# Optimization experiments

Measured on AMD Instinct MI355X. Metric: run time of the kernel, lower is better.

Reference implementation:

```python
import jax, jax.numpy as jnp
import numpy as np

F = 39          # total fields = 13 numeric + 26 categorical
NUM_NUM = 13
N_CAT = 26
V = 100000      # vocab per categorical field
E = 16          # embed size
RED = max(1, F // 3)  # SE reduction size = 13
P = F * (F - 1) // 2  # 741 pairs
HID = [1024, 512, 256]
B = 4096

I_IDX, J_IDX = np.triu_indices(F, k=1)  # static pair indices, len P


def setup_inputs() -> dict:
    key = jax.random.key(0)
    ks = jax.random.split(key, 16)
    s = 0.01
    inp = {
        "cat": jax.random.randint(ks[0], (B, N_CAT), 0, V),
        "num": jax.random.normal(ks[1], (B, NUM_NUM), dtype=jnp.float32),
        "embed_tables": jax.random.normal(ks[2], (N_CAT, V, E), dtype=jnp.float32) * s,
        "num_emb": jax.random.normal(ks[3], (NUM_NUM, E), dtype=jnp.float32) * s,
        "W_se1": jax.random.normal(ks[4], (F, RED), dtype=jnp.float32) * 0.1,
        "W_se2": jax.random.normal(ks[5], (RED, F), dtype=jnp.float32) * 0.1,
        "W_bil": jax.random.normal(ks[6], (F, E, E), dtype=jnp.float32) * 0.1,  # per-field Linear(E,E,no bias), [field,in,out]
        "W_d1": jax.random.normal(ks[7], (2 * P * E, HID[0]), dtype=jnp.float32) * 0.01,
        "b_d1": jnp.zeros((HID[0],), dtype=jnp.float32),
        "W_d2": jax.random.normal(ks[8], (HID[0], HID[1]), dtype=jnp.float32) * 0.02,
        "b_d2": jnp.zeros((HID[1],), dtype=jnp.float32),
        "W_d3": jax.random.normal(ks[9], (HID[1], HID[2]), dtype=jnp.float32) * 0.02,
        "b_d3": jnp.zeros((HID[2],), dtype=jnp.float32),
        "W_out": jax.random.normal(ks[10], (HID[2], 1), dtype=jnp.float32) * 0.02,
        "b_out": jnp.zeros((1,), dtype=jnp.float32),
    }
    return inp


def _bilinear_each(x, W_bil):
    # x: [B,F,E]; project each field with its own matrix, then pairwise multiply.
    proj = jnp.einsum("bfe,fed->bfd", x, W_bil)            # [B,F,E]
    return proj[:, I_IDX, :] * x[:, J_IDX, :]               # [B,P,E]


def reference(cat, num, embed_tables, num_emb, W_se1, W_se2, W_bil,
              W_d1, b_d1, W_d2, b_d2, W_d3, b_d3, W_out, b_out):
    # categorical embeddings: per-field gather -> [B, N_CAT, E]
    cat_embed = embed_tables[jnp.arange(N_CAT)[None, :], cat]
    # numerical "embeddings": value * learned vector -> [B, NUM_NUM, E]
    num_embed = num[:, :, None] * num_emb[None, :, :]
    x = jnp.concatenate([num_embed, cat_embed], axis=1)     # [B,F,E]

    # SENET gating
    Z = jnp.mean(x, axis=-1)                                 # [B,F]
    A = jax.nn.relu(jax.nn.relu(Z @ W_se1) @ W_se2)          # [B,F]
    V = x * A[:, :, None]

    se_bi = _bilinear_each(V, W_bil)                         # [B,P,E]
    bi = _bilinear_each(x, W_bil)                            # [B,P,E]
    hid = jnp.concatenate([se_bi, bi], axis=1).reshape(x.shape[0], -1)  # [B, 2*P*E]

    h = jax.nn.relu(hid @ W_d1 + b_d1)
    h = jax.nn.relu(h @ W_d2 + b_d2)
    h = jax.nn.relu(h @ W_d3 + b_d3)
    return h @ W_out + b_out                                 # [B,1]
```

## Files before the change

### kernel.cpp

```cpp
#include <hip/hip_runtime.h>

typedef unsigned short u16;
typedef __attribute__((ext_vector_type(8))) __bf16 bf16x8;
typedef __attribute__((ext_vector_type(4))) float f32x4;

#define NF    39
#define NNUM  13
#define NCAT  26
#define VOC   100000
#define NPAIR 741
#define KHID  23712
#define BATCH 4096
#define HD1   1024
#define HD2   512
#define HD3   256

__device__ __forceinline__ u16 f2bf(float f) {
  unsigned u = __builtin_bit_cast(unsigned, f);
  return (u16)((u + 0x7fffu + ((u >> 16) & 1u)) >> 16);
}

__device__ __forceinline__ void gload16(const void* g, void* l) {
  __builtin_amdgcn_global_load_lds((const __attribute__((address_space(1))) void*)g,
                                   (__attribute__((address_space(3))) void*)l, 16, 0, 0);
}

__global__ __launch_bounds__(256) void fuse_front(
    const int* __restrict__ cat, const float* __restrict__ num,
    const float* __restrict__ tables, const float* __restrict__ nemb,
    const float* __restrict__ Wse1, const float* __restrict__ Wse2,
    const float* __restrict__ Wbil, u16* __restrict__ hid)
{
  __shared__ float xs[NF][16];
  __shared__ float wb[NF][16][16];
  __shared__ float pr[NF][16];
  __shared__ float Zs[NF], Ts[NNUM], As[NF];
  __shared__ unsigned char pis[NPAIR], pjs[NPAIR];

  const int b = blockIdx.x;
  const int tid = threadIdx.x;

  for (int i = tid; i < NF * 256; i += 256) ((float*)wb)[i] = Wbil[i];

  for (int t = tid; t < NNUM * 16; t += 256) {
    int f = t >> 4, e = t & 15;
    xs[f][e] = num[b * NNUM + f] * nemb[t];
  }
  for (int t = tid; t < NCAT * 16; t += 256) {
    int c = t >> 4, e = t & 15;
    int cv = cat[b * NCAT + c];
    xs[NNUM + c][e] = tables[((size_t)c * VOC + cv) * 16 + e];
  }
  for (int p = tid; p < NPAIR; p += 256) {
    int i = 0, rs = 0;
    while (p >= rs + (NF - 1 - i)) { rs += NF - 1 - i; ++i; }
    pis[p] = (unsigned char)i;
    pjs[p] = (unsigned char)(i + 1 + (p - rs));
  }
  __syncthreads();

  if (tid < NF) {
    float s = 0.f;
    #pragma unroll
    for (int e = 0; e < 16; ++e) s += xs[tid][e];
    Zs[tid] = s * (1.f / 16.f);
  }
  __syncthreads();
  if (tid < NNUM) {
    float s = 0.f;
    for (int f = 0; f < NF; ++f) s += Zs[f] * Wse1[f * NNUM + tid];
    Ts[tid] = fmaxf(s, 0.f);
  }
  __syncthreads();
  if (tid < NF) {
    float s = 0.f;
    for (int r = 0; r < NNUM; ++r) s += Ts[r] * Wse2[r * NF + tid];
    As[tid] = fmaxf(s, 0.f);
  }
  for (int t = tid; t < NF * 16; t += 256) {
    int f = t >> 4, d = t & 15;
    float s = 0.f;
    #pragma unroll
    for (int e = 0; e < 16; ++e) s += xs[f][e] * wb[f][e][d];
    pr[f][d] = s;
  }
  __syncthreads();

  u16* hr = hid + (size_t)b * KHID;
  for (int idx = tid; idx < NPAIR * 16; idx += 256) {
    int p = idx >> 4, e = idx & 15;
    int i = pis[p], j = pjs[p];
    float bv = pr[i][e] * xs[j][e];
    hr[NPAIR * 16 + idx] = f2bf(bv);
    hr[idx] = f2bf(As[i] * As[j] * bv);
  }
}

__global__ __launch_bounds__(256) void transpose_cast(
    const float* __restrict__ in, u16* __restrict__ out, int K, int N)
{
  __shared__ float t[32][33];
  const int k0 = blockIdx.x * 32, n0 = blockIdx.y * 32;
  const int c = threadIdx.x & 31, r = threadIdx.x >> 5;
  #pragma unroll
  for (int it = 0; it < 4; ++it)
    t[r + it * 8][c] = in[(size_t)(k0 + r + it * 8) * N + n0 + c];
  __syncthreads();
  #pragma unroll
  for (int it = 0; it < 4; ++it)
    out[(size_t)(n0 + r + it * 8) * K + k0 + c] = f2bf(t[c][r + it * 8]);
}

__global__ __launch_bounds__(512, 2) void gemm8p_bf16(
    const u16* __restrict__ A, const u16* __restrict__ Bt,
    float* __restrict__ Cp, int M, int N, int K, int totku, int kpb)
{
  __shared__ __align__(16) u16 lds[65536];

  const int tid = threadIdx.x;
  const int wid = tid >> 6, lane = tid & 63;

  const int d = blockIdx.x;
  const int x = d & 7, jj = d >> 3;
  const int mb = ((x & 3) << 2) | (jj & 3);
  const int nb = (jj >> 2) & 3;
  const int sb = ((x >> 2) << 1) | (jj >> 4);

  const int ks0 = sb * kpb;
  const int kunits = (totku - ks0 < kpb) ? (totku - ks0) : kpb;
  const int ftiles = kunits >> 1;

  const int wm = wid >> 2, wn = wid & 3;
  const int lrow = lane & 15, c0 = lane >> 4;

  const int rr = tid >> 2, cc = tid & 3, csrc = cc ^ ((rr >> 1) & 3);
  const u16* pAg = A  + (size_t)((size_t)mb * 256 + rr) * K + (size_t)ks0 * 32 + csrc * 8;
  const u16* pBg = Bt + (size_t)((size_t)nb * 256 + rr) * K + (size_t)ks0 * 32 + csrc * 8;
  const size_t rsk = (size_t)128 * K;
  const int dstoff = tid * 8;

  int offA[8], offB[4];
  #pragma unroll
  for (int m = 0; m < 8; ++m) {
    int r = wm * 128 + m * 16 + lrow;
    offA[m] = r * 32 + ((c0 ^ ((r >> 1) & 3)) << 3);
  }
  #pragma unroll
  for (int n = 0; n < 4; ++n) {
    int r = wn * 64 + n * 16 + lrow;
    offB[n] = r * 32 + ((c0 ^ ((r >> 1) & 3)) << 3);
  }

#define STAGE_A(g) { int sg = ((g) < kunits) ? (g) : (kunits - 1);          \
    const u16* s_ = pAg + (size_t)sg * 32;                                   \
    u16* dp_ = lds + (((g) & 3) * 8192) + dstoff;                            \
    gload16(s_, dp_); gload16(s_ + rsk, dp_ + 4096); }
#define STAGE_B(g) { int sg = ((g) < kunits) ? (g) : (kunits - 1);          \
    const u16* s_ = pBg + (size_t)sg * 32;                                   \
    u16* dp_ = lds + 32768 + (((g) & 3) * 8192) + dstoff;                    \
    gload16(s_, dp_); gload16(s_ + rsk, dp_ + 4096); }

  f32x4 acc[8][4];
  #pragma unroll
  for (int m = 0; m < 8; ++m)
    #pragma unroll
    for (int n = 0; n < 4; ++n) acc[m][n] = f32x4{0.f, 0.f, 0.f, 0.f};

  STAGE_A(0); STAGE_B(0); STAGE_A(1); STAGE_B(1); STAGE_A(2); STAGE_B(2); STAGE_B(3);
  asm volatile("s_waitcnt vmcnt(10)" ::: "memory");
  __builtin_amdgcn_s_barrier();

  bf16x8 a0, a1, a2, a3, bg0, bg1, bg2, bg3;

  for (int tt = 0; tt < ftiles; ++tt) {
    const int g0 = tt << 1;
    const u16* As0 = lds + ((g0 & 3) * 8192);
    const u16* As1 = lds + (((g0 + 1) & 3) * 8192);
    const u16* Bs0 = lds + 32768 + ((g0 & 3) * 8192);
    const u16* Bs1 = lds + 32768 + (((g0 + 1) & 3) * 8192);

    a0 = *reinterpret_cast<const bf16x8*>(As0 + offA[0]);
    a1 = *reinterpret_cast<const bf16x8*>(As0 + offA[1]);
    a2 = *reinterpret_cast<const bf16x8*>(As0 + offA[2]);
    a3 = *reinterpret_cast<const bf16x8*>(As0 + offA[3]);
    bg0 = *reinterpret_cast<const bf16x8*>(Bs0 + offB[0]);
    bg1 = *reinterpret_cast<const bf16x8*>(Bs0 + offB[1]);
    bg2 = *reinterpret_cast<const bf16x8*>(Bs0 + offB[2]);
    bg3 = *reinterpret_cast<const bf16x8*>(Bs0 + offB[3]);
    STAGE_A(g0 + 3);
    __builtin_amdgcn_sched_barrier(0);
    __builtin_amdgcn_s_barrier();
    asm volatile("s_waitcnt lgkmcnt(0)" ::: "memory");
    __builtin_amdgcn_sched_barrier(0);
    __builtin_amdgcn_s_setprio(1);
    acc[0][0] = __builtin_amdgcn_mfma_f32_16x16x32_bf16(a0, bg0, acc[0][0], 0, 0, 0);
    acc[0][1] = __builtin_amdgcn_mfma_f32_16x16x32_bf16(a0, bg1, acc[0][1], 0, 0, 0);
    acc[0][2] = __builtin_amdgcn_mfma_f32_16x16x32_bf16(a0, bg2, acc[0][2], 0, 0, 0);
    acc[0][3] = __builtin_amdgcn_mfma_f32_16x16x32_bf16(a0, bg3, acc[0][3], 0, 0, 0);
    acc[1][0] = __builtin_amdgcn_mfma_f32_16x16x32_bf16(a1, bg0, acc[1][0], 0, 0, 0);
    acc[1][1] = __builtin_amdgcn_mfma_f32_16x16x32_bf16(a1, bg1, acc[1][1], 0, 0, 0);
    acc[1][2] = __builtin_amdgcn_mfma_f32_16x16x32_bf16(a1, bg2, acc[1][2], 0, 0, 0);
    acc[1][3] = __builtin_amdgcn_mfma_f32_16x16x32_bf16(a1, bg3, acc[1][3], 0, 0, 0);
    acc[2][0] = __builtin_amdgcn_mfma_f32_16x16x32_bf16(a2, bg0, acc[2][0], 0, 0, 0);
    acc[2][1] = __builtin_amdgcn_mfma_f32_16x16x32_bf16(a2, bg1, acc[2][1], 0, 0, 0);
    acc[2][2] = __builtin_amdgcn_mfma_f32_16x16x32_bf16(a2, bg2, acc[2][2], 0, 0, 0);
    acc[2][3] = __builtin_amdgcn_mfma_f32_16x16x32_bf16(a2, bg3, acc[2][3], 0, 0, 0);
    acc[3][0] = __builtin_amdgcn_mfma_f32_16x16x32_bf16(a3, bg0, acc[3][0], 0, 0, 0);
    acc[3][1] = __builtin_amdgcn_mfma_f32_16x16x32_bf16(a3, bg1, acc[3][1], 0, 0, 0);
    acc[3][2] = __builtin_amdgcn_mfma_f32_16x16x32_bf16(a3, bg2, acc[3][2], 0, 0, 0);
    acc[3][3] = __builtin_amdgcn_mfma_f32_16x16x32_bf16(a3, bg3, acc[3][3], 0, 0, 0);
    __builtin_amdgcn_s_setprio(0);
    __builtin_amdgcn_sched_barrier(0);
    __builtin_amdgcn_s_barrier();

    a0 = *reinterpret_cast<const bf16x8*>(As0 + offA[4]);
    a1 = *reinterpret_cast<const bf16x8*>(As0 + offA[5]);
    a2 = *reinterpret_cast<const bf16x8*>(As0 + offA[6]);
    a3 = *reinterpret_cast<const bf16x8*>(As0 + offA[7]);
    STAGE_B(g0 + 4);
    __builtin_amdgcn_sched_barrier(0);
    __builtin_amdgcn_s_barrier();
    asm volatile("s_waitcnt lgkmcnt(0)" ::: "memory");
    __builtin_amdgcn_sched_barrier(0);
    __builtin_amdgcn_s_setprio(1);
    acc[4][0] = __builtin_amdgcn_mfma_f32_16x16x32_bf16(a0, bg0, acc[4][0], 0, 0, 0);
    acc[4][1] = __builtin_amdgcn_mfma_f32_16x16x32_bf16(a0, bg1, acc[4][1], 0, 0, 0);
    acc[4][2] = __builtin_amdgcn_mfma_f32_16x16x32_bf16(a0, bg2, acc[4][2], 0, 0, 0);
    acc[4][3] = __builtin_amdgcn_mfma_f32_16x16x32_bf16(a0, bg3, acc[4][3], 0, 0, 0);
    acc[5][0] = __builtin_amdgcn_mfma_f32_16x16x32_bf16(a1, bg0, acc[5][0], 0, 0, 0);
    acc[5][1] = __builtin_amdgcn_mfma_f32_16x16x32_bf16(a1, bg1, acc[5][1], 0, 0, 0);
    acc[5][2] = __builtin_amdgcn_mfma_f32_16x16x32_bf16(a1, bg2, acc[5][2], 0, 0, 0);
    acc[5][3] = __builtin_amdgcn_mfma_f32_16x16x32_bf16(a1, bg3, acc[5][3], 0, 0, 0);
    acc[6][0] = __builtin_amdgcn_mfma_f32_16x16x32_bf16(a2, bg0, acc[6][0], 0, 0, 0);
    acc[6][1] = __builtin_amdgcn_mfma_f32_16x16x32_bf16(a2, bg1, acc[6][1], 0, 0, 0);
    acc[6][2] = __builtin_amdgcn_mfma_f32_16x16x32_bf16(a2, bg2, acc[6][2], 0, 0, 0);
    acc[6][3] = __builtin_amdgcn_mfma_f32_16x16x32_bf16(a2, bg3, acc[6][3], 0, 0, 0);
    acc[7][0] = __builtin_amdgcn_mfma_f32_16x16x32_bf16(a3, bg0, acc[7][0], 0, 0, 0);
    acc[7][1] = __builtin_amdgcn_mfma_f32_16x16x32_bf16(a3, bg1, acc[7][1], 0, 0, 0);
    acc[7][2] = __builtin_amdgcn_mfma_f32_16x16x32_bf16(a3, bg2, acc[7][2], 0, 0, 0);
    acc[7][3] = __builtin_amdgcn_mfma_f32_16x16x32_bf16(a3, bg3, acc[7][3], 0, 0, 0);
    __builtin_amdgcn_s_setprio(0);
    __builtin_amdgcn_sched_barrier(0);
    asm volatile("s_waitcnt vmcnt(8)" ::: "memory");
    __builtin_amdgcn_s_barrier();

    a0 = *reinterpret_cast<const bf16x8*>(As1 + offA[0]);
    a1 = *reinterpret_cast<const bf16x8*>(As1 + offA[1]);
    a2 = *reinterpret_cast<const bf16x8*>(As1 + offA[2]);
    a3 = *reinterpret_cast<const bf16x8*>(As1 + offA[3]);
    bg0 = *reinterpret_cast<const bf16x8*>(Bs1 + offB[0]);
    bg1 = *reinterpret_cast<const bf16x8*>(Bs1 + offB[1]);
    bg2 = *reinterpret_cast<const bf16x8*>(Bs1 + offB[2]);
    bg3 = *reinterpret_cast<const bf16x8*>(Bs1 + offB[3]);
    STAGE_A(g0 + 4);
    __builtin_amdgcn_sched_barrier(0);
    __builtin_amdgcn_s_barrier();
    asm volatile("s_waitcnt lgkmcnt(0)" ::: "memory");
    __builtin_amdgcn_sched_barrier(0);
    __builtin_amdgcn_s_setprio(1);
    acc[0][0] = __builtin_amdgcn_mfma_f32_16x16x32_bf16(a0, bg0, acc[0][0], 0, 0, 0);
    acc[0][1] = __builtin_amdgcn_mfma_f32_16x16x32_bf16(a0, bg1, acc[0][1], 0, 0, 0);
    acc[0][2] = __builtin_amdgcn_mfma_f32_16x16x32_bf16(a0, bg2, acc[0][2], 0, 0, 0);
    acc[0][3] = __builtin_amdgcn_mfma_f32_16x16x32_bf16(a0, bg3, acc[0][3], 0, 0, 0);
    acc[1][0] = __builtin_amdgcn_mfma_f32_16x16x32_bf16(a1, bg0, acc[1][0], 0, 0, 0);
    acc[1][1] = __builtin_amdgcn_mfma_f32_16x16x32_bf16(a1, bg1, acc[1][1], 0, 0, 0);
    acc[1][2] = __builtin_amdgcn_mfma_f32_16x16x32_bf16(a1, bg2, acc[1][2], 0, 0, 0);
    acc[1][3] = __builtin_amdgcn_mfma_f32_16x16x32_bf16(a1, bg3, acc[1][3], 0, 0, 0);
    acc[2][0] = __builtin_amdgcn_mfma_f32_16x16x32_bf16(a2, bg0, acc[2][0], 0, 0, 0);
    acc[2][1] = __builtin_amdgcn_mfma_f32_16x16x32_bf16(a2, bg1, acc[2][1], 0, 0, 0);
    acc[2][2] = __builtin_amdgcn_mfma_f32_16x16x32_bf16(a2, bg2, acc[2][2], 0, 0, 0);
    acc[2][3] = __builtin_amdgcn_mfma_f32_16x16x32_bf16(a2, bg3, acc[2][3], 0, 0, 0);
    acc[3][0] = __builtin_amdgcn_mfma_f32_16x16x32_bf16(a3, bg0, acc[3][0], 0, 0, 0);
    acc[3][1] = __builtin_amdgcn_mfma_f32_16x16x32_bf16(a3, bg1, acc[3][1], 0, 0, 0);
    acc[3][2] = __builtin_amdgcn_mfma_f32_16x16x32_bf16(a3, bg2, acc[3][2], 0, 0, 0);
    acc[3][3] = __builtin_amdgcn_mfma_f32_16x16x32_bf16(a3, bg3, acc[3][3], 0, 0, 0);
    __builtin_amdgcn_s_setprio(0);
    __builtin_amdgcn_sched_barrier(0);
    __builtin_amdgcn_s_barrier();

    a0 = *reinterpret_cast<const bf16x8*>(As1 + offA[4]);
    a1 = *reinterpret_cast<const bf16x8*>(As1 + offA[5]);
    a2 = *reinterpret_cast<const bf16x8*>(As1 + offA[6]);
    a3 = *reinterpret_cast<const bf16x8*>(As1 + offA[7]);
    STAGE_B(g0 + 5);
    __builtin_amdgcn_sched_barrier(0);
    __builtin_amdgcn_s_barrier();
    asm volatile("s_waitcnt lgkmcnt(0)" ::: "memory");
    __builtin_amdgcn_sched_barrier(0);
    __builtin_amdgcn_s_setprio(1);
    acc[4][0] = __builtin_amdgcn_mfma_f32_16x16x32_bf16(a0, bg0, acc[4][0], 0, 0, 0);
    acc[4][1] = __builtin_amdgcn_mfma_f32_16x16x32_bf16(a0, bg1, acc[4][1], 0, 0, 0);
    acc[4][2] = __builtin_amdgcn_mfma_f32_16x16x32_bf16(a0, bg2, acc[4][2], 0, 0, 0);
    acc[4][3] = __builtin_amdgcn_mfma_f32_16x16x32_bf16(a0, bg3, acc[4][3], 0, 0, 0);
    acc[5][0] = __builtin_amdgcn_mfma_f32_16x16x32_bf16(a1, bg0, acc[5][0], 0, 0, 0);
    acc[5][1] = __builtin_amdgcn_mfma_f32_16x16x32_bf16(a1, bg1, acc[5][1], 0, 0, 0);
    acc[5][2] = __builtin_amdgcn_mfma_f32_16x16x32_bf16(a1, bg2, acc[5][2], 0, 0, 0);
    acc[5][3] = __builtin_amdgcn_mfma_f32_16x16x32_bf16(a1, bg3, acc[5][3], 0, 0, 0);
    acc[6][0] = __builtin_amdgcn_mfma_f32_16x16x32_bf16(a2, bg0, acc[6][0], 0, 0, 0);
    acc[6][1] = __builtin_amdgcn_mfma_f32_16x16x32_bf16(a2, bg1, acc[6][1], 0, 0, 0);
    acc[6][2] = __builtin_amdgcn_mfma_f32_16x16x32_bf16(a2, bg2, acc[6][2], 0, 0, 0);
    acc[6][3] = __builtin_amdgcn_mfma_f32_16x16x32_bf16(a2, bg3, acc[6][3], 0, 0, 0);
    acc[7][0] = __builtin_amdgcn_mfma_f32_16x16x32_bf16(a3, bg0, acc[7][0], 0, 0, 0);
    acc[7][1] = __builtin_amdgcn_mfma_f32_16x16x32_bf16(a3, bg1, acc[7][1], 0, 0, 0);
    acc[7][2] = __builtin_amdgcn_mfma_f32_16x16x32_bf16(a3, bg2, acc[7][2], 0, 0, 0);
    acc[7][3] = __builtin_amdgcn_mfma_f32_16x16x32_bf16(a3, bg3, acc[7][3], 0, 0, 0);
    __builtin_amdgcn_s_setprio(0);
    __builtin_amdgcn_sched_barrier(0);
    asm volatile("s_waitcnt vmcnt(8)" ::: "memory");
    __builtin_amdgcn_s_barrier();
  }

  if (kunits & 1) {
    asm volatile("s_waitcnt vmcnt(0)" ::: "memory");
    __builtin_amdgcn_s_barrier();
    const int g = kunits - 1;
    const u16* As = lds + ((g & 3) * 8192);
    const u16* Bs = lds + 32768 + ((g & 3) * 8192);
    bg0 = *reinterpret_cast<const bf16x8*>(Bs + offB[0]);
    bg1 = *reinterpret_cast<const bf16x8*>(Bs + offB[1]);
    bg2 = *reinterpret_cast<const bf16x8*>(Bs + offB[2]);
    bg3 = *reinterpret_cast<const bf16x8*>(Bs + offB[3]);
    #pragma unroll
    for (int m = 0; m < 8; ++m) {
      bf16x8 am = *reinterpret_cast<const bf16x8*>(As + offA[m]);
      acc[m][0] = __builtin_amdgcn_mfma_f32_16x16x32_bf16(am, bg0, acc[m][0], 0, 0, 0);
      acc[m][1] = __builtin_amdgcn_mfma_f32_16x16x32_bf16(am, bg1, acc[m][1], 0, 0, 0);
      acc[m][2] = __builtin_amdgcn_mfma_f32_16x16x32_bf16(am, bg2, acc[m][2], 0, 0, 0);
      acc[m][3] = __builtin_amdgcn_mfma_f32_16x16x32_bf16(am, bg3, acc[m][3], 0, 0, 0);
    }
  }
#undef STAGE_A
#undef STAGE_B

  float* C = Cp + (size_t)sb * M * N;
  #pragma unroll
  for (int m = 0; m < 8; ++m) {
    const int rb = mb * 256 + wm * 128 + m * 16 + (lane >> 4) * 4;
    #pragma unroll
    for (int n = 0; n < 4; ++n) {
      const int col = nb * 256 + wn * 64 + n * 16 + (lane & 15);
      #pragma unroll
      for (int j2 = 0; j2 < 4; ++j2)
        __builtin_nontemporal_store(acc[m][n][j2], &C[(size_t)(rb + j2) * N + col]);
    }
  }
}

__global__ __launch_bounds__(256) void gemm_bf16(
    const u16* __restrict__ A, const u16* __restrict__ Bt,
    float* __restrict__ Cp, int M, int N, int K, int kps)
{
  __shared__ __align__(16) u16 lA[128 * 32];
  __shared__ __align__(16) u16 lB[128 * 32];
  const int tid = threadIdx.x;
  const int mb = blockIdx.x, nb = blockIdx.y, sb = blockIdx.z;
  const int w = tid >> 6, lane = tid & 63;
  const int wr = (w >> 1) * 64, wc = (w & 1) * 64;
  const int lrow = lane & 15, lko = (lane >> 4) * 8;

  f32x4 acc[4][4];
  #pragma unroll
  for (int m = 0; m < 4; ++m)
    #pragma unroll
    for (int n = 0; n < 4; ++n) acc[m][n] = f32x4{0.f, 0.f, 0.f, 0.f};

  const u16* Ab = A + (size_t)mb * 128 * K;
  const u16* Bb = Bt + (size_t)nb * 128 * K;
  const int r0 = tid >> 2, inn = (tid & 3) * 8;
  const int l0 = (tid & ~63) * 8, l1 = ((256 + tid) & ~63) * 8;

  const int ks1 = (sb + 1) * kps;
  for (int ks = sb * kps; ks < ks1; ++ks) {
    const int k0 = ks * 32;
    __syncthreads();
    gload16(Ab + (size_t)r0 * K + k0 + inn,        lA + l0);
    gload16(Ab + (size_t)(r0 + 64) * K + k0 + inn, lA + l1);
    gload16(Bb + (size_t)r0 * K + k0 + inn,        lB + l0);
    gload16(Bb + (size_t)(r0 + 64) * K + k0 + inn, lB + l1);
    __syncthreads();
    bf16x8 af[4], bg[4];
    #pragma unroll
    for (int m = 0; m < 4; ++m)
      af[m] = *reinterpret_cast<const bf16x8*>(&lA[(wr + m * 16 + lrow) * 32 + lko]);
    #pragma unroll
    for (int n = 0; n < 4; ++n)
      bg[n] = *reinterpret_cast<const bf16x8*>(&lB[(wc + n * 16 + lrow) * 32 + lko]);
    #pragma unroll
    for (int m = 0; m < 4; ++m)
      #pragma unroll
      for (int n = 0; n < 4; ++n)
        acc[m][n] = __builtin_amdgcn_mfma_f32_16x16x32_bf16(af[m], bg[n], acc[m][n], 0, 0, 0);
  }

  float* C = Cp + (size_t)sb * M * N;
  #pragma unroll
  for (int m = 0; m < 4; ++m) {
    const int rb = mb * 128 + wr + m * 16 + (lane >> 4) * 4;
    #pragma unroll
    for (int n = 0; n < 4; ++n) {
      const int col = nb * 128 + wc + n * 16 + (lane & 15);
      #pragma unroll
      for (int j = 0; j < 4; ++j)
        __builtin_nontemporal_store(acc[m][n][j], &C[(size_t)(rb + j) * N + col]);
    }
  }
}

__global__ __launch_bounds__(256) void reduce_bias_relu_bf16(
    const float* __restrict__ part, int S, size_t MN,
    const float* __restrict__ bias, int nmask, u16* __restrict__ out)
{
  for (size_t i = blockIdx.x * 256ull + threadIdx.x; i < MN; i += (size_t)gridDim.x * 256) {
    float s = 0.f;
    for (int k = 0; k < S; ++k) s += __builtin_nontemporal_load(&part[(size_t)k * MN + i]);
    s += bias[i & nmask];
    out[i] = f2bf(fmaxf(s, 0.f));
  }
}

__global__ __launch_bounds__(256) void reduce_bias_relu_f32(
    const float* __restrict__ part, int S, size_t MN,
    const float* __restrict__ bias, int nmask, float* __restrict__ out)
{
  for (size_t i = blockIdx.x * 256ull + threadIdx.x; i < MN; i += (size_t)gridDim.x * 256) {
    float s = 0.f;
    for (int k = 0; k < S; ++k) s += __builtin_nontemporal_load(&part[(size_t)k * MN + i]);
    s += bias[i & nmask];
    out[i] = fmaxf(s, 0.f);
  }
}

__global__ __launch_bounds__(256) void final_dot(
    const float* __restrict__ h3, const float* __restrict__ Wout,
    const float* __restrict__ bout, float* __restrict__ out)
{
  const int row = blockIdx.x * 4 + (threadIdx.x >> 6);
  const int lane = threadIdx.x & 63;
  const float* hr = h3 + (size_t)row * HD3;
  float s = 0.f;
  #pragma unroll
  for (int i = 0; i < 4; ++i) s += hr[lane + i * 64] * Wout[lane + i * 64];
  #pragma unroll
  for (int off = 32; off; off >>= 1) s += __shfl_down(s, off, 64);
  if (lane == 0) out[row] = s + bout[0];
}

extern "C" void kernel_launch(void* const* d_in, const int* in_sizes, int n_in,
                              void* d_out, int out_size, void* d_ws, size_t ws_size,
                              hipStream_t stream)
{
  const int*   cat    = (const int*)  d_in[0];
  const float* num    = (const float*)d_in[1];
  const float* tables = (const float*)d_in[2];
  const float* nemb   = (const float*)d_in[3];
  const float* Wse1   = (const float*)d_in[4];
  const float* Wse2   = (const float*)d_in[5];
  const float* Wbil   = (const float*)d_in[6];
  const float* Wd1    = (const float*)d_in[7];
  const float* bd1    = (const float*)d_in[8];
  const float* Wd2    = (const float*)d_in[9];
  const float* bd2    = (const float*)d_in[10];
  const float* Wd3    = (const float*)d_in[11];
  const float* bd3    = (const float*)d_in[12];
  const float* Wout   = (const float*)d_in[13];
  const float* bout   = (const float*)d_in[14];

  char* ws = (char*)d_ws;
  u16*   hid  = (u16*)  (ws + 0ull);
  u16*   W1t  = (u16*)  (ws + 194248704ull);
  float* part = (float*)(ws + 242810880ull);
  u16*   W2t  = (u16*)  (ws + 309919744ull);
  u16*   W3t  = (u16*)  (ws + 310968320ull);
  u16*   h1b  = (u16*)  (ws + 0ull);
  u16*   h2b  = (u16*)  (ws + 8388608ull);
  float* h3f  = (float*)(ws + 12582912ull);

  transpose_cast<<<dim3(KHID / 32, HD1 / 32), 256, 0, stream>>>(Wd1, W1t, KHID, HD1);
  transpose_cast<<<dim3(HD1 / 32, HD2 / 32), 256, 0, stream>>>(Wd2, W2t, HD1, HD2);
  transpose_cast<<<dim3(HD2 / 32, HD3 / 32), 256, 0, stream>>>(Wd3, W3t, HD2, HD3);
  fuse_front<<<BATCH, 256, 0, stream>>>(cat, num, tables, nemb, Wse1, Wse2, Wbil, hid);

  gemm8p_bf16<<<256, 512, 0, stream>>>(hid, W1t, part, BATCH, HD1, KHID, 741, 186);
  reduce_bias_relu_bf16<<<2048, 256, 0, stream>>>(part, 4, (size_t)BATCH * HD1, bd1, HD1 - 1, h1b);

  gemm_bf16<<<dim3(BATCH / 128, HD2 / 128, 2), 256, 0, stream>>>(h1b, W2t, part, BATCH, HD2, HD1, 16);
  reduce_bias_relu_bf16<<<2048, 256, 0, stream>>>(part, 2, (size_t)BATCH * HD2, bd2, HD2 - 1, h2b);

  gemm_bf16<<<dim3(BATCH / 128, HD3 / 128, 4), 256, 0, stream>>>(h2b, W3t, part, BATCH, HD3, HD2, 4);
  reduce_bias_relu_f32<<<2048, 256, 0, stream>>>(part, 4, (size_t)BATCH * HD3, bd3, HD3 - 1, h3f);

  final_dot<<<BATCH / 4, 256, 0, stream>>>(h3f, Wout, bout, (float*)d_out);
}
```

Before: 365.0 us.

## Vectorize memory ops in front, transpose, and reduce kernels; merge transposes

Several memory-bound kernels switch to wider accesses. fuse_front loads W_bil with 16-byte loads and writes 8 bf16 per thread. The three weight transposes are merged into one launch that writes 4 bf16 per store. The reduce kernels handle 8 elements per thread with float4 loads, and two of them use smaller grids. The aim is fewer memory instructions, better coalesced stores and fewer kernel launches, at the cost of assuming sizes divisible by 8 and aligned pointers.

```diff
diff --git a/kernel.cpp b/kernel.cpp
--- a/kernel.cpp
+++ b/kernel.cpp
@@ -3,6 +3,8 @@
 typedef unsigned short u16;
 typedef __attribute__((ext_vector_type(8))) __bf16 bf16x8;
 typedef __attribute__((ext_vector_type(4))) float f32x4;
+typedef __attribute__((ext_vector_type(4))) unsigned short u16x4;
+typedef __attribute__((ext_vector_type(8))) unsigned short u16x8;
 
 #define NF    39
 #define NNUM  13
@@ -40,7 +42,8 @@
   const int b = blockIdx.x;
   const int tid = threadIdx.x;
 
-  for (int i = tid; i < NF * 256; i += 256) ((float*)wb)[i] = Wbil[i];
+  for (int i = tid; i < NF * 64; i += 256)
+    ((f32x4*)wb)[i] = ((const f32x4*)Wbil)[i];
 
   for (int t = tid; t < NNUM * 16; t += 256) {
     int f = t >> 4, e = t & 15;
@@ -87,28 +90,45 @@
   __syncthreads();
 
   u16* hr = hid + (size_t)b * KHID;
-  for (int idx = tid; idx < NPAIR * 16; idx += 256) {
-    int p = idx >> 4, e = idx & 15;
-    int i = pis[p], j = pjs[p];
-    float bv = pr[i][e] * xs[j][e];
-    hr[NPAIR * 16 + idx] = f2bf(bv);
-    hr[idx] = f2bf(As[i] * As[j] * bv);
-  }
-}
-
-__global__ __launch_bounds__(256) void transpose_cast(
-    const float* __restrict__ in, u16* __restrict__ out, int K, int N)
+  for (int idx2 = tid; idx2 < NPAIR * 2; idx2 += 256) {
+    const int p = idx2 >> 1, e0 = (idx2 & 1) * 8;
+    const int i = pis[p], j = pjs[p];
+    const float aa = As[i] * As[j];
+    u16x8 vb, vs;
+    #pragma unroll
+    for (int e = 0; e < 8; ++e) {
+      float bv = pr[i][e0 + e] * xs[j][e0 + e];
+      vb[e] = f2bf(bv);
+      vs[e] = f2bf(aa * bv);
+    }
+    *reinterpret_cast<u16x8*>(hr + NPAIR * 16 + p * 16 + e0) = vb;
+    *reinterpret_cast<u16x8*>(hr + p * 16 + e0) = vs;
+  }
+}
+
+__global__ __launch_bounds__(256) void transpose_all(
+    const float* __restrict__ Wd1, const float* __restrict__ Wd2,
+    const float* __restrict__ Wd3, u16* __restrict__ W1t,
+    u16* __restrict__ W2t, u16* __restrict__ W3t)
 {
   __shared__ float t[32][33];
-  const int k0 = blockIdx.x * 32, n0 = blockIdx.y * 32;
+  const int bid = blockIdx.x;
+  const float* in; u16* out; int K, N, kb, nb;
+  if (bid < 741 * 32)        { in = Wd1; out = W1t; K = KHID; N = HD1; kb = bid % 741; nb = bid / 741; }
+  else if (bid < 741 * 32 + 512) { int r = bid - 741 * 32; in = Wd2; out = W2t; K = HD1; N = HD2; kb = r % 32; nb = r / 32; }
+  else                       { int r = bid - 741 * 32 - 512; in = Wd3; out = W3t; K = HD2; N = HD3; kb = r % 16; nb = r / 16; }
+
+  const int k0 = kb * 32, n0 = nb * 32;
   const int c = threadIdx.x & 31, r = threadIdx.x >> 5;
   #pragma unroll
   for (int it = 0; it < 4; ++it)
     t[r + it * 8][c] = in[(size_t)(k0 + r + it * 8) * N + n0 + c];
   __syncthreads();
-  #pragma unroll
-  for (int it = 0; it < 4; ++it)
-    out[(size_t)(n0 + r + it * 8) * K + k0 + c] = f2bf(t[c][r + it * 8]);
+  const int n = threadIdx.x >> 3, kq = (threadIdx.x & 7) * 4;
+  u16x4 v;
+  #pragma unroll
+  for (int q = 0; q < 4; ++q) v[q] = f2bf(t[kq + q][n]);
+  *reinterpret_cast<u16x4*>(out + (size_t)(n0 + n) * K + k0 + kq) = v;
 }
 
 __global__ __launch_bounds__(512, 2) void gemm8p_bf16(
@@ -410,11 +430,25 @@
     const float* __restrict__ part, int S, size_t MN,
     const float* __restrict__ bias, int nmask, u16* __restrict__ out)
 {
-  for (size_t i = blockIdx.x * 256ull + threadIdx.x; i < MN; i += (size_t)gridDim.x * 256) {
-    float s = 0.f;
-    for (int k = 0; k < S; ++k) s += __builtin_nontemporal_load(&part[(size_t)k * MN + i]);
-    s += bias[i & nmask];
-    out[i] = f2bf(fmaxf(s, 0.f));
+  const size_t n8 = MN >> 3;
+  for (size_t i8 = blockIdx.x * 256ull + threadIdx.x; i8 < n8; i8 += (size_t)gridDim.x * 256) {
+    const size_t base = i8 * 8;
+    f32x4 lo = {0.f, 0.f, 0.f, 0.f}, hi = {0.f, 0.f, 0.f, 0.f};
+    for (int k = 0; k < S; ++k) {
+      const float* p = part + (size_t)k * MN + base;
+      f32x4 a = __builtin_nontemporal_load(reinterpret_cast<const f32x4*>(p));
+      f32x4 b = __builtin_nontemporal_load(reinterpret_cast<const f32x4*>(p + 4));
+      lo += a; hi += b;
+    }
+    const int bb = (int)(base & (size_t)nmask);
+    const f32x4 b0 = *reinterpret_cast<const f32x4*>(bias + bb);
+    const f32x4 b1 = *reinterpret_cast<const f32x4*>(bias + bb + 4);
+    u16x8 v;
+    #pragma unroll
+    for (int e = 0; e < 4; ++e) v[e] = f2bf(fmaxf(lo[e] + b0[e], 0.f));
+    #pragma unroll
+    for (int e = 0; e < 4; ++e) v[4 + e] = f2bf(fmaxf(hi[e] + b1[e], 0.f));
+    *reinterpret_cast<u16x8*>(out + base) = v;
   }
 }
 
@@ -422,11 +456,24 @@
     const float* __restrict__ part, int S, size_t MN,
     const float* __restrict__ bias, int nmask, float* __restrict__ out)
 {
-  for (size_t i = blockIdx.x * 256ull + threadIdx.x; i < MN; i += (size_t)gridDim.x * 256) {
-    float s = 0.f;
-    for (int k = 0; k < S; ++k) s += __builtin_nontemporal_load(&part[(size_t)k * MN + i]);
-    s += bias[i & nmask];
-    out[i] = fmaxf(s, 0.f);
+  const size_t n8 = MN >> 3;
+  for (size_t i8 = blockIdx.x * 256ull + threadIdx.x; i8 < n8; i8 += (size_t)gridDim.x * 256) {
+    const size_t base = i8 * 8;
+    f32x4 lo = {0.f, 0.f, 0.f, 0.f}, hi = {0.f, 0.f, 0.f, 0.f};
+    for (int k = 0; k < S; ++k) {
+      const float* p = part + (size_t)k * MN + base;
+      f32x4 a = __builtin_nontemporal_load(reinterpret_cast<const f32x4*>(p));
+      f32x4 b = __builtin_nontemporal_load(reinterpret_cast<const f32x4*>(p + 4));
+      lo += a; hi += b;
+    }
+    const int bb = (int)(base & (size_t)nmask);
+    const f32x4 b0 = *reinterpret_cast<const f32x4*>(bias + bb);
+    const f32x4 b1 = *reinterpret_cast<const f32x4*>(bias + bb + 4);
+    f32x4 o0, o1;
+    #pragma unroll
+    for (int e = 0; e < 4; ++e) { o0[e] = fmaxf(lo[e] + b0[e], 0.f); o1[e] = fmaxf(hi[e] + b1[e], 0.f); }
+    *reinterpret_cast<f32x4*>(out + base) = o0;
+    *reinterpret_cast<f32x4*>(out + base + 4) = o1;
   }
 }
 
@@ -475,19 +522,17 @@
   u16*   h2b  = (u16*)  (ws + 8388608ull);
   float* h3f  = (float*)(ws + 12582912ull);
 
-  transpose_cast<<<dim3(KHID / 32, HD1 / 32), 256, 0, stream>>>(Wd1, W1t, KHID, HD1);
-  transpose_cast<<<dim3(HD1 / 32, HD2 / 32), 256, 0, stream>>>(Wd2, W2t, HD1, HD2);
-  transpose_cast<<<dim3(HD2 / 32, HD3 / 32), 256, 0, stream>>>(Wd3, W3t, HD2, HD3);
+  transpose_all<<<741 * 32 + 512 + 128, 256, 0, stream>>>(Wd1, Wd2, Wd3, W1t, W2t, W3t);
   fuse_front<<<BATCH, 256, 0, stream>>>(cat, num, tables, nemb, Wse1, Wse2, Wbil, hid);
 
   gemm8p_bf16<<<256, 512, 0, stream>>>(hid, W1t, part, BATCH, HD1, KHID, 741, 186);
   reduce_bias_relu_bf16<<<2048, 256, 0, stream>>>(part, 4, (size_t)BATCH * HD1, bd1, HD1 - 1, h1b);
 
   gemm_bf16<<<dim3(BATCH / 128, HD2 / 128, 2), 256, 0, stream>>>(h1b, W2t, part, BATCH, HD2, HD1, 16);
-  reduce_bias_relu_bf16<<<2048, 256, 0, stream>>>(part, 2, (size_t)BATCH * HD2, bd2, HD2 - 1, h2b);
+  reduce_bias_relu_bf16<<<1024, 256, 0, stream>>>(part, 2, (size_t)BATCH * HD2, bd2, HD2 - 1, h2b);
 
   gemm_bf16<<<dim3(BATCH / 128, HD3 / 128, 4), 256, 0, stream>>>(h2b, W3t, part, BATCH, HD3, HD2, 4);
-  reduce_bias_relu_f32<<<2048, 256, 0, stream>>>(part, 4, (size_t)BATCH * HD3, bd3, HD3 - 1, h3f);
+  reduce_bias_relu_f32<<<512, 256, 0, stream>>>(part, 4, (size_t)BATCH * HD3, bd3, HD3 - 1, h3f);
 
   final_dot<<<BATCH / 4, 256, 0, stream>>>(h3f, Wout, bout, (float*)d_out);
 }
```

Result: faster. 343.2 us (-6.0%).
